# Kernel optimization log

Measured on AMD Instinct MI355X. Metric: run time of the kernel, lower is better.

## Reference

```python
import jax, jax.numpy as jnp
import numpy as np

B, C, T = 8, 512, 4096
KC, VC, H = 512, 512, 1  # key_channels, value_channels, num_heads
SCALE = KC // (H ** 0.5)  # faithful to original: key_channels // num_heads**0.5


def setup_inputs() -> dict:
    key = jax.random.key(0)
    k1, k2, k3, k4, k5 = jax.random.split(key, 5)
    x = jax.random.normal(k1, (B, C, T), dtype=jnp.float32)
    # 1x1 Conv1d weights: Conv1d(C, out, kernel_size=1) == per-timestep Linear
    Wqk = jax.random.normal(k2, (KC, C), dtype=jnp.float32) / np.sqrt(C)
    bqk = jax.random.normal(k3, (KC,), dtype=jnp.float32) * 0.01
    Wv = jax.random.normal(k4, (VC, C), dtype=jnp.float32) / np.sqrt(C)
    bv = jax.random.normal(k5, (VC,), dtype=jnp.float32) * 0.01
    return {"x": x, "Wqk": Wqk, "bqk": bqk, "Wv": Wv, "bv": bv}


def reference(x, Wqk, bqk, Wv, bv):
    # 1x1 conv projections: [B,C,T] -> [B,K,T] / [B,V,T]
    qk = jnp.einsum('kc,bct->bkt', Wqk, x) + bqk[None, :, None]
    val = jnp.einsum('vc,bct->bvt', Wv, x) + bv[None, :, None]
    # channel-wise attention: with num_heads=1 the reshape/transpose/matmul
    # chain reduces to scores[b,k,v] = sum_t qk[b,k,t] * val[b,v,t]
    scores = jnp.einsum('bkt,bvt->bkv', qk, val) / SCALE
    p = jax.nn.softmax(scores, axis=-1)          # softmax over value channels
    # inference path: dropout is identity (self.training == False)
    out = jnp.einsum('bkv,bvt->bkt', p, val)     # [B,K,T], K == input_channels
    return out.reshape(-1, C, T)
```

## Files before the change

kernel.cpp:

```cpp
#include <hip/hip_runtime.h>
#include <hip/hip_bf16.h>


#define BB 8
#define CC 512
#define TT 4096

typedef __attribute__((ext_vector_type(8))) short bf16x8;
typedef __attribute__((ext_vector_type(4))) short bf16x4;
typedef __attribute__((ext_vector_type(4))) float f32x4;

__device__ __forceinline__ void gload_lds16(const void* g, void* l) {
  __builtin_amdgcn_global_load_lds((const __attribute__((address_space(1))) void*)g,
                                   (__attribute__((address_space(3))) void*)l,
                                   16, 0, 0);
}
__device__ __forceinline__ float bf2f(short u) {
  return __uint_as_float(((unsigned)(unsigned short)u) << 16);
}
__device__ __forceinline__ unsigned short f2bf(float f) {
  return __builtin_bit_cast(unsigned short, __float2bfloat16(f));
}

__global__ __launch_bounds__(256)
void convert_stream_kernel(const float* __restrict__ x, __hip_bfloat16* __restrict__ xh,
                           float* __restrict__ sx)
{
  const int gid = blockIdx.x * 256 + threadIdx.x;
#pragma unroll
  for (int it = 0; it < 4; it++) {
    const int chunk = it * 524288 + gid;
    const size_t base = (size_t)chunk * 8;
    const float4 a = *(const float4*)&x[base];
    const float4 c = *(const float4*)&x[base + 4];
    bf16x8 h;
    h[0] = (short)f2bf(a.x); h[1] = (short)f2bf(a.y);
    h[2] = (short)f2bf(a.z); h[3] = (short)f2bf(a.w);
    h[4] = (short)f2bf(c.x); h[5] = (short)f2bf(c.y);
    h[6] = (short)f2bf(c.z); h[7] = (short)f2bf(c.w);
    *(bf16x8*)&xh[base] = h;
    float s = ((a.x + a.y) + (a.z + a.w)) + ((c.x + c.y) + (c.z + c.w));
#pragma unroll
    for (int off = 32; off; off >>= 1) s += __shfl_xor(s, off);
    if ((threadIdx.x & 63) == 0) atomicAdd(&sx[chunk >> 9], s);
  }
}

__global__ __launch_bounds__(256)
void convert_w_kernel(const float* __restrict__ Wqk, const float* __restrict__ Wv,
                      __hip_bfloat16* __restrict__ Wqkh, __hip_bfloat16* __restrict__ Wvh,
                      __hip_bfloat16* __restrict__ WvT)
{
  int i = blockIdx.x * 256 + threadIdx.x;
  Wqkh[i] = __float2bfloat16(Wqk[i]);
  float wv = Wv[i];
  Wvh[i] = __float2bfloat16(wv);
  WvT[(i & 511) * 512 + (i >> 9)] = __float2bfloat16(wv);
}

__global__ __launch_bounds__(256)
void tatb_kernel(const float* __restrict__ Wqk, const float* __restrict__ Wv,
                 const float* __restrict__ sx, float* __restrict__ ta, float* __restrict__ tb)
{
  int wid = threadIdx.x >> 6, lane = threadIdx.x & 63;
  int gid = blockIdx.x * 4 + wid;
  int which = gid >> 12;
  int rem = gid & 4095;
  int b = rem >> 9, j = rem & 511;
  const float* W = which ? Wv : Wqk;
  float s = 0.f;
#pragma unroll
  for (int i = 0; i < 8; i++) {
    int c = lane + i * 64;
    s += W[j * 512 + c] * sx[b * 512 + c];
  }
#pragma unroll
  for (int off = 32; off; off >>= 1) s += __shfl_xor(s, off);
  if (lane == 0) (which ? tb : ta)[b * 512 + j] = s;
}

template <int BM, int BN, int EPI>
__global__ __launch_bounds__(256)
void gemm_nt_kernel(const __hip_bfloat16* __restrict__ A, long strideA, int ldA,
                    const __hip_bfloat16* __restrict__ B, long strideB, int ldB,
                    void* __restrict__ C, long strideC, int ldC,
                    int Kslice, int nslices,
                    const float* __restrict__ p1, const float* __restrict__ p2,
                    const float* __restrict__ p3, const float* __restrict__ p4)
{
  constexpr int FM = BM / 32, FN = BN / 32;
  const int tid = threadIdx.x, lane = tid & 63, wid = tid >> 6;

  const int gx = gridDim.x, gy = gridDim.y;
  const int lin = blockIdx.x + gx * (blockIdx.y + gy * blockIdx.z);
  const int nwg = gx * gy * (int)gridDim.z;
  const int lin2 = (lin & 7) * (nwg >> 3) + (lin >> 3);
  const int tn = lin2 % gx;
  const int r1 = lin2 / gx;
  const int tm = r1 % gy;
  const int z  = r1 / gy;
  const int b  = z / nslices;
  const int ks = z - b * nslices;

  const __hip_bfloat16* Ab = A + (size_t)b * strideA + (size_t)(tm * BM) * ldA + (size_t)ks * Kslice;
  const __hip_bfloat16* Bb = B + (size_t)b * strideB + (size_t)(tn * BN) * ldB + (size_t)ks * Kslice;

  __shared__ __align__(16) __hip_bfloat16 sA[2][BM * 64];
  __shared__ __align__(16) __hip_bfloat16 sB[2][BN * 64];

  const int wr = wid >> 1, wc = wid & 1;

  f32x4 acc[FM][FN];
#pragma unroll
  for (int m = 0; m < FM; m++)
#pragma unroll
    for (int n = 0; n < FN; n++) acc[m][n] = (f32x4){0.f, 0.f, 0.f, 0.f};

  auto stage = [&](int buf, int k0) {
#pragma unroll
    for (int i = 0; i < BM / 32; i++) {
      int e = tid * 8 + i * 2048;
      int row = e >> 6, colg = (e & 63) ^ ((row & 7) << 3);
      gload_lds16(Ab + (size_t)row * ldA + k0 + colg, &sA[buf][wid * 512 + i * 2048]);
    }
#pragma unroll
    for (int i = 0; i < BN / 32; i++) {
      int e = tid * 8 + i * 2048;
      int row = e >> 6, colg = (e & 63) ^ ((row & 7) << 3);
      gload_lds16(Bb + (size_t)row * ldB + k0 + colg, &sB[buf][wid * 512 + i * 2048]);
    }
  };

  stage(0, 0);
  __syncthreads();
  const int nsteps = Kslice >> 6;
  for (int s = 0; s < nsteps; s++) {
    if (s + 1 < nsteps) stage((s + 1) & 1, (s + 1) << 6);
    const __hip_bfloat16* cA = sA[s & 1];
    const __hip_bfloat16* cB = sB[s & 1];
#pragma unroll
    for (int ks2 = 0; ks2 < 2; ks2++) {
      bf16x8 af[FM], bfv[FN];
      const int kb = ks2 * 32 + (lane >> 4) * 8;
#pragma unroll
      for (int m = 0; m < FM; m++) {
        int row = wr * (BM / 2) + m * 16 + (lane & 15);
        af[m] = *(const bf16x8*)&cA[row * 64 + (kb ^ ((row & 7) << 3))];
      }
#pragma unroll
      for (int n = 0; n < FN; n++) {
        int row = wc * (BN / 2) + n * 16 + (lane & 15);
        bfv[n] = *(const bf16x8*)&cB[row * 64 + (kb ^ ((row & 7) << 3))];
      }
#pragma unroll
      for (int m = 0; m < FM; m++)
#pragma unroll
        for (int n = 0; n < FN; n++)
          acc[m][n] = __builtin_amdgcn_mfma_f32_16x16x32_bf16(af[m], bfv[n], acc[m][n], 0, 0, 0);
    }
    __syncthreads();
  }

  const int rb = tm * BM + wr * (BM / 2) + ((lane >> 4) << 2);
  const int cb = tn * BN + wc * (BN / 2) + (lane & 15);

  if (EPI == 0) {
    __hip_bfloat16* Cb = (__hip_bfloat16*)C + (size_t)z * strideC;
#pragma unroll
    for (int m = 0; m < FM; m++)
#pragma unroll
      for (int n = 0; n < FN; n++)
#pragma unroll
        for (int r = 0; r < 4; r++) {
          int row = rb + m * 16 + r, col = cb + n * 16;
          Cb[(size_t)row * ldC + col] = __float2bfloat16(acc[m][n][r]);
        }
  } else if (EPI == 1) {
    float* Cf = (float*)C + (size_t)z * strideC;
    const float* ta = p3 + b * 512;
    const float* tb = p4 + b * 512;
#pragma unroll
    for (int m = 0; m < FM; m++)
#pragma unroll
      for (int n = 0; n < FN; n++)
#pragma unroll
        for (int r = 0; r < 4; r++) {
          int row = rb + m * 16 + r, col = cb + n * 16;
          float bq = p1[row], bvv = p2[col];
          float v = acc[m][n][r] + bq * tb[col] + bvv * ta[row] + (float)TT * bq * bvv;
          Cf[(size_t)row * ldC + col] = v * (1.0f / 512.0f);
        }
  } else {
    float* Cf = (float*)C + (size_t)z * strideC;
    const float* pb = p1 + b * 512;
#pragma unroll
    for (int m = 0; m < FM; m++)
#pragma unroll
      for (int n = 0; n < FN; n++)
#pragma unroll
        for (int r = 0; r < 4; r++) {
          int row = rb + m * 16 + r, col = cb + n * 16;
          Cf[(size_t)row * ldC + col] = acc[m][n][r] + pb[row];
        }
  }
}

__global__ __launch_bounds__(256)
void reduce_g_kernel(const short* __restrict__ Gpart, short* __restrict__ Gb)
{
  const int idx = (blockIdx.x * 256 + threadIdx.x) * 8;
  const int b = idx >> 18, i = idx & 262143;
  const short* base = Gpart + ((size_t)(b * 4) << 18) + i;
  float s[8];
#pragma unroll
  for (int q = 0; q < 8; q++) s[q] = 0.f;
#pragma unroll
  for (int ks = 0; ks < 4; ks++) {
    bf16x8 v = *(const bf16x8*)(base + ((size_t)ks << 18));
#pragma unroll
    for (int q = 0; q < 8; q++) s[q] += bf2f(v[q]);
  }
  bf16x8 o;
#pragma unroll
  for (int q = 0; q < 8; q++) o[q] = (short)f2bf(s[q]);
  *(bf16x8*)(Gb + ((size_t)b << 18) + i) = o;
}

__global__ __launch_bounds__(256)
void softmax_kernel(const float* __restrict__ scores, const float* __restrict__ bv,
                    __hip_bfloat16* __restrict__ p, float* __restrict__ pb)
{
  const int row = blockIdx.x;
  const int tid = threadIdx.x;
  const float s0 = scores[(size_t)row * 512 + tid];
  const float s1 = scores[(size_t)row * 512 + 256 + tid];
  __shared__ float red[4];

  float m = fmaxf(s0, s1);
#pragma unroll
  for (int off = 32; off; off >>= 1) m = fmaxf(m, __shfl_xor(m, off));
  if ((tid & 63) == 0) red[tid >> 6] = m;
  __syncthreads();
  m = fmaxf(fmaxf(red[0], red[1]), fmaxf(red[2], red[3]));

  float e0 = __expf(s0 - m), e1 = __expf(s1 - m);
  float s = e0 + e1;
#pragma unroll
  for (int off = 32; off; off >>= 1) s += __shfl_xor(s, off);
  __syncthreads();
  if ((tid & 63) == 0) red[tid >> 6] = s;
  __syncthreads();
  s = red[0] + red[1] + red[2] + red[3];
  float inv = 1.0f / s;

  float p0 = e0 * inv, p1v = e1 * inv;
  p[(size_t)row * 512 + tid] = __float2bfloat16(p0);
  p[(size_t)row * 512 + 256 + tid] = __float2bfloat16(p1v);

  float contrib = p0 * bv[tid] + p1v * bv[256 + tid];
#pragma unroll
  for (int off = 32; off; off >>= 1) contrib += __shfl_xor(contrib, off);
  __syncthreads();
  if ((tid & 63) == 0) red[tid >> 6] = contrib;
  __syncthreads();
  if (tid == 0) pb[row] = red[0] + red[1] + red[2] + red[3];
}

__global__ __launch_bounds__(256)
void gemm_out_kernel(const __hip_bfloat16* __restrict__ Mall,
                     const __hip_bfloat16* __restrict__ xh,
                     const float* __restrict__ pball,
                     float* __restrict__ out)
{
  __shared__ __align__(16) __hip_bfloat16 sA[2][128 * 64];
  __shared__ __align__(16) __hip_bfloat16 sB[2][64 * 128];

  const int tid = threadIdx.x, lane = tid & 63, wid = tid >> 6;
  const int wr = wid >> 1, wc = wid & 1;

  const int lin = blockIdx.x + 32 * (blockIdx.y + 4 * blockIdx.z);
  const int lin2 = (lin & 7) * 128 + (lin >> 3);
  const int tn = lin2 & 31;
  const int tm = (lin2 >> 5) & 3;
  const int b  = lin2 >> 7;

  const __hip_bfloat16* Ab = Mall + (size_t)b * 262144 + (size_t)(tm * 128) * 512;
  const __hip_bfloat16* Bb = xh + (size_t)b * ((size_t)CC * TT) + tn * 128;

  f32x4 acc[4][4];
#pragma unroll
  for (int m = 0; m < 4; m++)
#pragma unroll
    for (int n = 0; n < 4; n++) acc[m][n] = (f32x4){0.f, 0.f, 0.f, 0.f};

  auto stage = [&](int buf, int k0) {
#pragma unroll
    for (int i = 0; i < 4; i++) {
      int e = tid * 8 + i * 2048;
      int row = e >> 6, colg = (e & 63) ^ ((row & 7) << 3);
      gload_lds16(Ab + (size_t)row * 512 + k0 + colg, &sA[buf][wid * 512 + i * 2048]);
    }
#pragma unroll
    for (int q = 0; q < 4; q++) {
      int E = q * 2048 + tid * 8;
      int v = ((E >> 9) << 2) | ((E >> 4) & 3);
      int t = (((E >> 6) & 7) << 4) | (E & 8);
      gload_lds16(Bb + (size_t)(k0 + v) * TT + t, &sB[buf][wid * 512 + q * 2048]);
    }
  };

  const unsigned sB32 =
      (unsigned)(size_t)(__attribute__((address_space(3))) __hip_bfloat16*)&sB[0][0];
  const unsigned btr_lo = sB32 + (lane >> 4) * 2048 + (lane & 15) * 8 + wc * 512;
  const unsigned btr_hi = btr_lo + 8192;

#define COMPUTE(BUF)                                                            \
  {                                                                             \
    _Pragma("unroll")                                                           \
    for (int ks2 = 0; ks2 < 2; ks2++) {                                         \
      bf16x8 af[4]; bf16x4 blo[4], bhi[4];                                      \
      const int kb = ks2 * 32 + (lane >> 4) * 8;                                \
      _Pragma("unroll")                                                         \
      for (int m = 0; m < 4; m++) {                                             \
        int row = wr * 64 + m * 16 + (lane & 15);                               \
        af[m] = *(const bf16x8*)&sA[BUF][row * 64 + (kb ^ ((row & 7) << 3))];   \
      }                                                                         \
      unsigned ab = ks2 ? btr_hi : btr_lo;                                      \
      _Pragma("unroll")                                                         \
      for (int n = 0; n < 4; n++) {                                             \
        asm volatile("ds_read_b64_tr_b16 %0, %1 offset:%2"                      \
                     : "=v"(blo[n]) : "v"(ab), "i"((BUF) * 16384 + n * 128));   \
        asm volatile("ds_read_b64_tr_b16 %0, %1 offset:%2"                      \
                     : "=v"(bhi[n]) : "v"(ab), "i"((BUF) * 16384 + n * 128 + 1024)); \
      }                                                                         \
      asm volatile("s_waitcnt lgkmcnt(0)" ::: "memory");                        \
      __builtin_amdgcn_sched_barrier(0);                                        \
      _Pragma("unroll")                                                         \
      for (int m = 0; m < 4; m++)                                               \
        _Pragma("unroll")                                                       \
        for (int n = 0; n < 4; n++) {                                           \
          bf16x8 b8 = __builtin_shufflevector(blo[n], bhi[n], 0, 1, 2, 3, 4, 5, 6, 7); \
          acc[m][n] = __builtin_amdgcn_mfma_f32_16x16x32_bf16(af[m], b8, acc[m][n], 0, 0, 0); \
        }                                                                       \
    }                                                                           \
  }

  stage(0, 0);
  __syncthreads();
#pragma unroll 1
  for (int s = 0; s < 8; s += 2) {
    if (s + 1 < 8) stage(1, (s + 1) * 64);
    COMPUTE(0);
    __syncthreads();
    if (s + 2 < 8) stage(0, (s + 2) * 64);
    COMPUTE(1);
    __syncthreads();
  }
#undef COMPUTE

  const int rb = tm * 128 + wr * 64 + ((lane >> 4) << 2);
  const int cb = tn * 128 + wc * 64 + (lane & 15);
  float* Cf = out + (size_t)b * ((size_t)CC * TT);
  const float* pb = pball + b * 512;
#pragma unroll
  for (int m = 0; m < 4; m++)
#pragma unroll
    for (int n = 0; n < 4; n++)
#pragma unroll
      for (int r = 0; r < 4; r++) {
        int row = rb + m * 16 + r, col = cb + n * 16;
        Cf[(size_t)row * TT + col] = acc[m][n][r] + pb[row];
      }
}

extern "C" void kernel_launch(void* const* d_in, const int* in_sizes, int n_in,
                              void* d_out, int out_size, void* d_ws, size_t ws_size,
                              hipStream_t stream)
{
  const float* x   = (const float*)d_in[0];
  const float* Wqk = (const float*)d_in[1];
  const float* bqk = (const float*)d_in[2];
  const float* Wv  = (const float*)d_in[3];
  const float* bv  = (const float*)d_in[4];
  float* out = (float*)d_out;

  char* w = (char*)d_ws;
  auto alloc = [&](size_t bytes) {
    void* pp = (void*)w;
    w += (bytes + 255) & ~(size_t)255;
    return pp;
  };
  __hip_bfloat16* xh     = (__hip_bfloat16*)alloc((size_t)BB * CC * TT * 2);
  short*          Gpart  = (short*)alloc((size_t)BB * 4 * CC * CC * 2);
  short*          Gb     = (short*)alloc((size_t)BB * CC * CC * 2);
  __hip_bfloat16* S2     = (__hip_bfloat16*)alloc((size_t)BB * CC * CC * 2);
  float*          scores = (float*)alloc((size_t)BB * CC * CC * 4);
  __hip_bfloat16* pmat   = (__hip_bfloat16*)alloc((size_t)BB * CC * CC * 2);
  __hip_bfloat16* Mm     = (__hip_bfloat16*)alloc((size_t)BB * CC * CC * 2);
  __hip_bfloat16* Wqkh   = (__hip_bfloat16*)alloc((size_t)CC * CC * 2);
  __hip_bfloat16* Wvh    = (__hip_bfloat16*)alloc((size_t)CC * CC * 2);
  __hip_bfloat16* WvT    = (__hip_bfloat16*)alloc((size_t)CC * CC * 2);
  float* sx = (float*)alloc((size_t)BB * CC * 4);
  float* ta = (float*)alloc((size_t)BB * CC * 4);
  float* tb = (float*)alloc((size_t)BB * CC * 4);
  float* pb = (float*)alloc((size_t)BB * CC * 4);

  hipMemsetAsync(sx, 0, (size_t)BB * CC * 4, stream);

  convert_stream_kernel<<<2048, 256, 0, stream>>>(x, xh, sx);
  convert_w_kernel<<<(CC * CC) / 256, 256, 0, stream>>>(Wqk, Wv, Wqkh, Wvh, WvT);
  tatb_kernel<<<(2 * BB * CC) / 4, 256, 0, stream>>>(Wqk, Wv, sx, ta, tb);

  const long sXH = (long)CC * TT;
  const long sSq = (long)CC * CC;

  gemm_nt_kernel<128, 128, 0><<<dim3(4, 4, BB * 4), 256, 0, stream>>>(
      xh, sXH, TT, xh, sXH, TT, Gpart, sSq, CC, 1024, 4,
      nullptr, nullptr, nullptr, nullptr);
  reduce_g_kernel<<<(BB * CC * CC) / (256 * 8), 256, 0, stream>>>(Gpart, Gb);

  gemm_nt_kernel<64, 64, 0><<<dim3(8, 8, BB), 256, 0, stream>>>(
      Wvh, 0, CC, (const __hip_bfloat16*)Gb, sSq, CC, S2, sSq, CC, 512, 1,
      nullptr, nullptr, nullptr, nullptr);

  gemm_nt_kernel<64, 64, 1><<<dim3(8, 8, BB), 256, 0, stream>>>(
      Wqkh, 0, CC, S2, sSq, CC, scores, sSq, CC, 512, 1,
      bqk, bv, ta, tb);

  softmax_kernel<<<BB * CC, 256, 0, stream>>>(scores, bv, pmat, pb);

  gemm_nt_kernel<64, 64, 0><<<dim3(8, 8, BB), 256, 0, stream>>>(
      pmat, sSq, CC, WvT, 0, CC, Mm, sSq, CC, 512, 1,
      nullptr, nullptr, nullptr, nullptr);

  gemm_out_kernel<<<dim3(32, 4, 8), 256, 0, stream>>>(Mm, xh, pb, out);
}
```

Baseline: 214.2 us.

## Fuse middle GEMM chain and softmax into one per-strip kernel

Replaces three 512x512 batched GEMMs plus the softmax kernel with a single middle_kernel. Each block owns a 32-row strip per batch and chains Wqk*G, then *Wv^T, then the bias epilogue, softmax, and P*WvT, keeping the intermediates in LDS. The weight conversion and ta/tb kernels are also merged into one launch. This removes several launches and the global round-trips of S2, scores and pmat. The trade-off is only 128 blocks, each using a large LDS footprint, so occupancy and parallelism are low and the serial staging loops are unpipelined.

Measured after the change: 215.2 us. Within noise of the previous version (+0.5%).

```diff
diff --git a/kernel.cpp b/kernel.cpp
--- a/kernel.cpp
+++ b/kernel.cpp
@@ -47,36 +47,36 @@
 }
 
 __global__ __launch_bounds__(256)
-void convert_w_kernel(const float* __restrict__ Wqk, const float* __restrict__ Wv,
-                      __hip_bfloat16* __restrict__ Wqkh, __hip_bfloat16* __restrict__ Wvh,
-                      __hip_bfloat16* __restrict__ WvT)
-{
-  int i = blockIdx.x * 256 + threadIdx.x;
-  Wqkh[i] = __float2bfloat16(Wqk[i]);
-  float wv = Wv[i];
-  Wvh[i] = __float2bfloat16(wv);
-  WvT[(i & 511) * 512 + (i >> 9)] = __float2bfloat16(wv);
-}
-
-__global__ __launch_bounds__(256)
-void tatb_kernel(const float* __restrict__ Wqk, const float* __restrict__ Wv,
-                 const float* __restrict__ sx, float* __restrict__ ta, float* __restrict__ tb)
-{
-  int wid = threadIdx.x >> 6, lane = threadIdx.x & 63;
-  int gid = blockIdx.x * 4 + wid;
-  int which = gid >> 12;
-  int rem = gid & 4095;
-  int b = rem >> 9, j = rem & 511;
-  const float* W = which ? Wv : Wqk;
-  float s = 0.f;
-#pragma unroll
-  for (int i = 0; i < 8; i++) {
-    int c = lane + i * 64;
-    s += W[j * 512 + c] * sx[b * 512 + c];
-  }
-#pragma unroll
-  for (int off = 32; off; off >>= 1) s += __shfl_xor(s, off);
-  if (lane == 0) (which ? tb : ta)[b * 512 + j] = s;
+void prep_w_kernel(const float* __restrict__ Wqk, const float* __restrict__ Wv,
+                   const float* __restrict__ sx,
+                   __hip_bfloat16* __restrict__ Wqkh, __hip_bfloat16* __restrict__ Wvh,
+                   __hip_bfloat16* __restrict__ WvT,
+                   float* __restrict__ ta, float* __restrict__ tb)
+{
+  const int blk = blockIdx.x;
+  if (blk < 1024) {
+    int i = blk * 256 + threadIdx.x;
+    Wqkh[i] = __float2bfloat16(Wqk[i]);
+    float wv = Wv[i];
+    Wvh[i] = __float2bfloat16(wv);
+    WvT[(i & 511) * 512 + (i >> 9)] = __float2bfloat16(wv);
+  } else {
+    int wid = threadIdx.x >> 6, lane = threadIdx.x & 63;
+    int gid = (blk - 1024) * 4 + wid;
+    int which = gid >> 12;
+    int rem = gid & 4095;
+    int b = rem >> 9, j = rem & 511;
+    const float* W = which ? Wv : Wqk;
+    float s = 0.f;
+#pragma unroll
+    for (int i2 = 0; i2 < 8; i2++) {
+      int c = lane + i2 * 64;
+      s += W[j * 512 + c] * sx[b * 512 + c];
+    }
+#pragma unroll
+    for (int off = 32; off; off >>= 1) s += __shfl_xor(s, off);
+    if (lane == 0) (which ? tb : ta)[b * 512 + j] = s;
+  }
 }
 
 template <int BM, int BN, int EPI>
@@ -84,9 +84,7 @@
 void gemm_nt_kernel(const __hip_bfloat16* __restrict__ A, long strideA, int ldA,
                     const __hip_bfloat16* __restrict__ B, long strideB, int ldB,
                     void* __restrict__ C, long strideC, int ldC,
-                    int Kslice, int nslices,
-                    const float* __restrict__ p1, const float* __restrict__ p2,
-                    const float* __restrict__ p3, const float* __restrict__ p4)
+                    int Kslice, int nslices)
 {
   constexpr int FM = BM / 32, FN = BN / 32;
   const int tid = threadIdx.x, lane = tid & 63, wid = tid >> 6;
@@ -163,46 +161,16 @@
 
   const int rb = tm * BM + wr * (BM / 2) + ((lane >> 4) << 2);
   const int cb = tn * BN + wc * (BN / 2) + (lane & 15);
-
-  if (EPI == 0) {
-    __hip_bfloat16* Cb = (__hip_bfloat16*)C + (size_t)z * strideC;
-#pragma unroll
-    for (int m = 0; m < FM; m++)
-#pragma unroll
-      for (int n = 0; n < FN; n++)
-#pragma unroll
-        for (int r = 0; r < 4; r++) {
-          int row = rb + m * 16 + r, col = cb + n * 16;
-          Cb[(size_t)row * ldC + col] = __float2bfloat16(acc[m][n][r]);
-        }
-  } else if (EPI == 1) {
-    float* Cf = (float*)C + (size_t)z * strideC;
-    const float* ta = p3 + b * 512;
-    const float* tb = p4 + b * 512;
-#pragma unroll
-    for (int m = 0; m < FM; m++)
-#pragma unroll
-      for (int n = 0; n < FN; n++)
-#pragma unroll
-        for (int r = 0; r < 4; r++) {
-          int row = rb + m * 16 + r, col = cb + n * 16;
-          float bq = p1[row], bvv = p2[col];
-          float v = acc[m][n][r] + bq * tb[col] + bvv * ta[row] + (float)TT * bq * bvv;
-          Cf[(size_t)row * ldC + col] = v * (1.0f / 512.0f);
-        }
-  } else {
-    float* Cf = (float*)C + (size_t)z * strideC;
-    const float* pb = p1 + b * 512;
-#pragma unroll
-    for (int m = 0; m < FM; m++)
-#pragma unroll
-      for (int n = 0; n < FN; n++)
-#pragma unroll
-        for (int r = 0; r < 4; r++) {
-          int row = rb + m * 16 + r, col = cb + n * 16;
-          Cf[(size_t)row * ldC + col] = acc[m][n][r] + pb[row];
-        }
-  }
+  __hip_bfloat16* Cb = (__hip_bfloat16*)C + (size_t)z * strideC;
+#pragma unroll
+  for (int m = 0; m < FM; m++)
+#pragma unroll
+    for (int n = 0; n < FN; n++)
+#pragma unroll
+      for (int r = 0; r < 4; r++) {
+        int row = rb + m * 16 + r, col = cb + n * 16;
+        Cb[(size_t)row * ldC + col] = __float2bfloat16(acc[m][n][r]);
+      }
 }
 
 __global__ __launch_bounds__(256)
@@ -227,43 +195,177 @@
 }
 
 __global__ __launch_bounds__(256)
-void softmax_kernel(const float* __restrict__ scores, const float* __restrict__ bv,
-                    __hip_bfloat16* __restrict__ p, float* __restrict__ pb)
-{
-  const int row = blockIdx.x;
-  const int tid = threadIdx.x;
-  const float s0 = scores[(size_t)row * 512 + tid];
-  const float s1 = scores[(size_t)row * 512 + 256 + tid];
-  __shared__ float red[4];
-
-  float m = fmaxf(s0, s1);
-#pragma unroll
-  for (int off = 32; off; off >>= 1) m = fmaxf(m, __shfl_xor(m, off));
-  if ((tid & 63) == 0) red[tid >> 6] = m;
+void middle_kernel(const __hip_bfloat16* __restrict__ Gh,
+                   const __hip_bfloat16* __restrict__ Wqkh,
+                   const __hip_bfloat16* __restrict__ Wvh,
+                   const __hip_bfloat16* __restrict__ WvT,
+                   const float* __restrict__ bqk, const float* __restrict__ bv,
+                   const float* __restrict__ ta, const float* __restrict__ tb,
+                   __hip_bfloat16* __restrict__ Mm, float* __restrict__ pb)
+{
+  __shared__ __align__(16) __hip_bfloat16 sW[32 * 512];
+  __shared__ __align__(16) __hip_bfloat16 sT[32 * 512];
+  __shared__ __align__(16) __hip_bfloat16 sB[512 * 64];
+  __shared__ float red1[4][32], red2[4][32], red3[4][32];
+
+  const int tid = threadIdx.x, lane = tid & 63, wid = tid >> 6;
+  const int strip = blockIdx.x, b = blockIdx.y;
+  const __hip_bfloat16* Ghb = Gh + (size_t)b * 262144;
+
+  {
+    const __hip_bfloat16* As = Wqkh + (size_t)(strip * 32) * 512;
+#pragma unroll
+    for (int i = 0; i < 8; i++) {
+      int row = i * 4 + wid;
+      int scol = (lane * 8) ^ ((row & 7) << 3);
+      gload_lds16(As + row * 512 + scol, &sW[i * 2048 + wid * 512]);
+    }
+  }
+
+  auto stageB = [&](const __hip_bfloat16* Bsrc, int k0) {
+    const int r0 = wid * 8 + (lane >> 3);
+    const int sc = k0 + 8 * ((lane & 7) ^ (lane >> 3));
+#pragma unroll
+    for (int i = 0; i < 16; i++)
+      gload_lds16(Bsrc + (size_t)(i * 32 + r0) * 512 + sc, &sB[i * 2048 + wid * 512]);
+  };
+
+  f32x4 acc[2][8];
+
+#define RUN_STAGE(BSRC, SX)                                                     \
+  {                                                                             \
+    _Pragma("unroll") for (int m = 0; m < 2; m++)                               \
+      _Pragma("unroll") for (int n = 0; n < 8; n++)                             \
+        acc[m][n] = (f32x4){0.f, 0.f, 0.f, 0.f};                                \
+    for (int t = 0; t < 8; t++) {                                               \
+      stageB(BSRC, t * 64);                                                     \
+      __syncthreads();                                                          \
+      _Pragma("unroll") for (int ks2 = 0; ks2 < 2; ks2++) {                     \
+        const int kb = ks2 * 32 + (lane >> 4) * 8;                              \
+        const int kq = t * 64 + kb;                                             \
+        bf16x8 af[2], bfr[8];                                                   \
+        _Pragma("unroll") for (int m = 0; m < 2; m++) {                         \
+          int row = m * 16 + (lane & 15);                                       \
+          af[m] = *(const bf16x8*)&SX[row * 512 + (kq ^ ((row & 7) << 3))];     \
+        }                                                                       \
+        _Pragma("unroll") for (int n = 0; n < 8; n++) {                         \
+          int row = wid * 128 + n * 16 + (lane & 15);                           \
+          bfr[n] = *(const bf16x8*)&sB[row * 64 + (kb ^ ((row & 7) << 3))];     \
+        }                                                                       \
+        _Pragma("unroll") for (int m = 0; m < 2; m++)                           \
+          _Pragma("unroll") for (int n = 0; n < 8; n++)                         \
+            acc[m][n] = __builtin_amdgcn_mfma_f32_16x16x32_bf16(af[m], bfr[n], acc[m][n], 0, 0, 0); \
+      }                                                                         \
+      __syncthreads();                                                          \
+    }                                                                           \
+  }
+
+  RUN_STAGE(Ghb, sW);
+#pragma unroll
+  for (int m = 0; m < 2; m++)
+#pragma unroll
+    for (int n = 0; n < 8; n++)
+#pragma unroll
+      for (int r = 0; r < 4; r++) {
+        int rowl = m * 16 + ((lane >> 4) << 2) + r;
+        int col = wid * 128 + n * 16 + (lane & 15);
+        sT[rowl * 512 + (col ^ ((rowl & 7) << 3))] = __float2bfloat16(acc[m][n][r]);
+      }
   __syncthreads();
-  m = fmaxf(fmaxf(red[0], red[1]), fmaxf(red[2], red[3]));
-
-  float e0 = __expf(s0 - m), e1 = __expf(s1 - m);
-  float s = e0 + e1;
-#pragma unroll
-  for (int off = 32; off; off >>= 1) s += __shfl_xor(s, off);
+
+  RUN_STAGE(Wvh, sT);
+
+  const float* tab = ta + b * 512;
+  const float* tbb = tb + b * 512;
+  float bq[2][4], tar[2][4], bvc[8], tbc[8];
+#pragma unroll
+  for (int m = 0; m < 2; m++)
+#pragma unroll
+    for (int r = 0; r < 4; r++) {
+      int row = strip * 32 + m * 16 + ((lane >> 4) << 2) + r;
+      bq[m][r] = bqk[row]; tar[m][r] = tab[row];
+    }
+#pragma unroll
+  for (int n = 0; n < 8; n++) {
+    int col = wid * 128 + n * 16 + (lane & 15);
+    bvc[n] = bv[col]; tbc[n] = tbb[col];
+  }
+#pragma unroll
+  for (int m = 0; m < 2; m++)
+#pragma unroll
+    for (int n = 0; n < 8; n++)
+#pragma unroll
+      for (int r = 0; r < 4; r++)
+        acc[m][n][r] = (acc[m][n][r] + bq[m][r] * tbc[n] + tar[m][r] * bvc[n]
+                        + 4096.0f * bq[m][r] * bvc[n]) * (1.0f / 512.0f);
+
+#pragma unroll
+  for (int m = 0; m < 2; m++)
+#pragma unroll
+    for (int r = 0; r < 4; r++) {
+      float v = acc[m][0][r];
+#pragma unroll
+      for (int n = 1; n < 8; n++) v = fmaxf(v, acc[m][n][r]);
+#pragma unroll
+      for (int off = 1; off < 16; off <<= 1) v = fmaxf(v, __shfl_xor(v, off));
+      if ((lane & 15) == 0) red1[wid][m * 16 + ((lane >> 4) << 2) + r] = v;
+    }
   __syncthreads();
-  if ((tid & 63) == 0) red[tid >> 6] = s;
+
+#pragma unroll
+  for (int m = 0; m < 2; m++)
+#pragma unroll
+    for (int r = 0; r < 4; r++) {
+      int lr = m * 16 + ((lane >> 4) << 2) + r;
+      float mx = fmaxf(fmaxf(red1[0][lr], red1[1][lr]), fmaxf(red1[2][lr], red1[3][lr]));
+      float s = 0.f, pbp = 0.f;
+#pragma unroll
+      for (int n = 0; n < 8; n++) {
+        float e = __expf(acc[m][n][r] - mx);
+        acc[m][n][r] = e;
+        s += e;
+        pbp += e * bvc[n];
+      }
+#pragma unroll
+      for (int off = 1; off < 16; off <<= 1) {
+        s += __shfl_xor(s, off);
+        pbp += __shfl_xor(pbp, off);
+      }
+      if ((lane & 15) == 0) { red2[wid][lr] = s; red3[wid][lr] = pbp; }
+    }
   __syncthreads();
-  s = red[0] + red[1] + red[2] + red[3];
-  float inv = 1.0f / s;
-
-  float p0 = e0 * inv, p1v = e1 * inv;
-  p[(size_t)row * 512 + tid] = __float2bfloat16(p0);
-  p[(size_t)row * 512 + 256 + tid] = __float2bfloat16(p1v);
-
-  float contrib = p0 * bv[tid] + p1v * bv[256 + tid];
-#pragma unroll
-  for (int off = 32; off; off >>= 1) contrib += __shfl_xor(contrib, off);
+
+#pragma unroll
+  for (int m = 0; m < 2; m++)
+#pragma unroll
+    for (int r = 0; r < 4; r++) {
+      int lr = m * 16 + ((lane >> 4) << 2) + r;
+      float inv = 1.0f / (red2[0][lr] + red2[1][lr] + red2[2][lr] + red2[3][lr]);
+      if (wid == 0 && (lane & 15) == 0)
+        pb[b * 512 + strip * 32 + lr] =
+            (red3[0][lr] + red3[1][lr] + red3[2][lr] + red3[3][lr]) * inv;
+#pragma unroll
+      for (int n = 0; n < 8; n++) {
+        int col = wid * 128 + n * 16 + (lane & 15);
+        sT[lr * 512 + (col ^ ((lr & 7) << 3))] = __float2bfloat16(acc[m][n][r] * inv);
+      }
+    }
   __syncthreads();
-  if ((tid & 63) == 0) red[tid >> 6] = contrib;
-  __syncthreads();
-  if (tid == 0) pb[row] = red[0] + red[1] + red[2] + red[3];
+
+  RUN_STAGE(WvT, sT);
+#undef RUN_STAGE
+
+  __hip_bfloat16* Mb = Mm + (size_t)b * 262144 + (size_t)(strip * 32) * 512;
+#pragma unroll
+  for (int m = 0; m < 2; m++)
+#pragma unroll
+    for (int n = 0; n < 8; n++)
+#pragma unroll
+      for (int r = 0; r < 4; r++) {
+        int rowl = m * 16 + ((lane >> 4) << 2) + r;
+        int col = wid * 128 + n * 16 + (lane & 15);
+        Mb[rowl * 512 + col] = __float2bfloat16(acc[m][n][r]);
+      }
 }
 
 __global__ __launch_bounds__(256)
@@ -361,7 +463,7 @@
   const int rb = tm * 128 + wr * 64 + ((lane >> 4) << 2);
   const int cb = tn * 128 + wc * 64 + (lane & 15);
   float* Cf = out + (size_t)b * ((size_t)CC * TT);
-  const float* pb = pball + b * 512;
+  const float* pbv = pball + b * 512;
 #pragma unroll
   for (int m = 0; m < 4; m++)
 #pragma unroll
@@ -369,7 +471,7 @@
 #pragma unroll
       for (int r = 0; r < 4; r++) {
         int row = rb + m * 16 + r, col = cb + n * 16;
-        Cf[(size_t)row * TT + col] = acc[m][n][r] + pb[row];
+        Cf[(size_t)row * TT + col] = acc[m][n][r] + pbv[row];
       }
 }
 
@@ -393,9 +495,6 @@
   __hip_bfloat16* xh     = (__hip_bfloat16*)alloc((size_t)BB * CC * TT * 2);
   short*          Gpart  = (short*)alloc((size_t)BB * 4 * CC * CC * 2);
   short*          Gb     = (short*)alloc((size_t)BB * CC * CC * 2);
-  __hip_bfloat16* S2     = (__hip_bfloat16*)alloc((size_t)BB * CC * CC * 2);
-  float*          scores = (float*)alloc((size_t)BB * CC * CC * 4);
-  __hip_bfloat16* pmat   = (__hip_bfloat16*)alloc((size_t)BB * CC * CC * 2);
   __hip_bfloat16* Mm     = (__hip_bfloat16*)alloc((size_t)BB * CC * CC * 2);
   __hip_bfloat16* Wqkh   = (__hip_bfloat16*)alloc((size_t)CC * CC * 2);
   __hip_bfloat16* Wvh    = (__hip_bfloat16*)alloc((size_t)CC * CC * 2);
@@ -408,30 +507,17 @@
   hipMemsetAsync(sx, 0, (size_t)BB * CC * 4, stream);
 
   convert_stream_kernel<<<2048, 256, 0, stream>>>(x, xh, sx);
-  convert_w_kernel<<<(CC * CC) / 256, 256, 0, stream>>>(Wqk, Wv, Wqkh, Wvh, WvT);
-  tatb_kernel<<<(2 * BB * CC) / 4, 256, 0, stream>>>(Wqk, Wv, sx, ta, tb);
+  prep_w_kernel<<<3072, 256, 0, stream>>>(Wqk, Wv, sx, Wqkh, Wvh, WvT, ta, tb);
 
   const long sXH = (long)CC * TT;
   const long sSq = (long)CC * CC;
 
   gemm_nt_kernel<128, 128, 0><<<dim3(4, 4, BB * 4), 256, 0, stream>>>(
-      xh, sXH, TT, xh, sXH, TT, Gpart, sSq, CC, 1024, 4,
-      nullptr, nullptr, nullptr, nullptr);
+      xh, sXH, TT, xh, sXH, TT, Gpart, sSq, CC, 1024, 4);
   reduce_g_kernel<<<(BB * CC * CC) / (256 * 8), 256, 0, stream>>>(Gpart, Gb);
 
-  gemm_nt_kernel<64, 64, 0><<<dim3(8, 8, BB), 256, 0, stream>>>(
-      Wvh, 0, CC, (const __hip_bfloat16*)Gb, sSq, CC, S2, sSq, CC, 512, 1,
-      nullptr, nullptr, nullptr, nullptr);
-
-  gemm_nt_kernel<64, 64, 1><<<dim3(8, 8, BB), 256, 0, stream>>>(
-      Wqkh, 0, CC, S2, sSq, CC, scores, sSq, CC, 512, 1,
-      bqk, bv, ta, tb);
-
-  softmax_kernel<<<BB * CC, 256, 0, stream>>>(scores, bv, pmat, pb);
-
-  gemm_nt_kernel<64, 64, 0><<<dim3(8, 8, BB), 256, 0, stream>>>(
-      pmat, sSq, CC, WvT, 0, CC, Mm, sSq, CC, 512, 1,
-      nullptr, nullptr, nullptr, nullptr);
+  middle_kernel<<<dim3(16, BB), 256, 0, stream>>>(
+      (const __hip_bfloat16*)Gb, Wqkh, Wvh, WvT, bqk, bv, ta, tb, Mm, pb);
 
   gemm_out_kernel<<<dim3(32, 4, 8), 256, 0, stream>>>(Mm, xh, pb, out);
 }
```
